# Kernel tuning notes

Hardware: AMD Instinct MI355X
Metric: run time of the kernel (lower is better)

## Reference

```python
import jax, jax.numpy as jnp
import numpy as np


def _maxpool2(x):
    # 2x2 max pool, stride 2; x: [B, C, H, W]
    B, C, H, W = x.shape
    return x.reshape(B, C, H // 2, 2, W // 2, 2).max(axis=(3, 5))


def setup_inputs() -> dict:
    key = jax.random.key(0)
    ks = jax.random.split(key, 6)
    B, C, H, W = 8, 256, 64, 64
    x = jax.random.normal(ks[0], (B, C, H, W), dtype=jnp.float32)
    w_theta = jax.random.normal(ks[1], (C // 8, C), dtype=jnp.float32) * (C ** -0.5)
    w_phi = jax.random.normal(ks[2], (C // 8, C), dtype=jnp.float32) * (C ** -0.5)
    w_g = jax.random.normal(ks[3], (C // 2, C), dtype=jnp.float32) * (C ** -0.5)
    w_o = jax.random.normal(ks[4], (C, C // 2), dtype=jnp.float32) * ((C // 2) ** -0.5)
    gamma = jnp.ones((), dtype=jnp.float32)
    return {"x": x, "w_theta": w_theta, "w_phi": w_phi, "w_g": w_g, "w_o": w_o, "gamma": gamma}


def reference(x, w_theta, w_phi, w_g, w_o, gamma):
    B, C, H, W = x.shape
    N = H * W
    # 1x1 convs are channel-mixing matmuls
    theta = jnp.einsum('oc,bchw->bohw', w_theta, x).reshape(B, C // 8, N)        # [B, C/8, N]
    phi = _maxpool2(jnp.einsum('oc,bchw->bohw', w_phi, x)).reshape(B, C // 8, N // 4)  # [B, C/8, N/4]
    g = _maxpool2(jnp.einsum('oc,bchw->bohw', w_g, x)).reshape(B, C // 2, N // 4)      # [B, C/2, N/4]
    # attention: softmax(theta^T phi) over pooled key axis
    beta = jax.nn.softmax(jnp.einsum('bcn,bcm->bnm', theta, phi), axis=-1)       # [B, N, N/4]
    o = jnp.einsum('bcm,bnm->bcn', g, beta).reshape(B, C // 2, H, W)             # [B, C/2, H, W]
    o = jnp.einsum('oc,bchw->bohw', w_o, o)                                      # [B, C, H, W]
    return gamma * o + x
```

## Files before the change

kernel.cpp:

```cpp
#include <hip/hip_runtime.h>

#define B_ 8
#define C_ 256
#define N_ 4096
#define CK 32
#define CG 128
#define M_ 1024

typedef __attribute__((ext_vector_type(8))) short bf16x8;
typedef __attribute__((ext_vector_type(4))) float f32x4;

__device__ __forceinline__ short f2bf(float f) {
  union { float f; unsigned u; } v; v.f = f;
  unsigned r = (v.u + 0x7FFF + ((v.u >> 16) & 1)) >> 16;
  return (short)r;
}
__device__ __forceinline__ int cvtpk(float lo, float hi) {
  int r;
  asm("v_cvt_pk_bf16_f32 %0, %1, %2" : "=v"(r) : "v"(lo), "v"(hi));
  return r;
}
__device__ __forceinline__ bf16x8 asbf(int4 v) {
  union { int4 i; bf16x8 b; } u; u.i = v; return u.b;
}
__device__ __forceinline__ void gload_lds16(const void* g, void* l) {
  __builtin_amdgcn_global_load_lds(
      (const __attribute__((address_space(1))) void*)g,
      (__attribute__((address_space(3))) void*)l, 16, 0, 0);
}

__global__ __launch_bounds__(512) void proj_kernel(const float* __restrict__ x,
                                                   const float* __restrict__ wt,
                                                   const float* __restrict__ wp,
                                                   const float* __restrict__ wg,
                                                   short* __restrict__ theta_t,
                                                   short* __restrict__ phi_t,
                                                   short* __restrict__ g_bf) {
  __shared__ __align__(16) short w_s[192 * 256];
  __shared__ __align__(16) short x_s[64 * 256];
  int tid = threadIdx.x;
  int bx = blockIdx.x, b = blockIdx.y;
  int t = bx >> 1, half = bx & 1;

#pragma unroll
  for (int rep = 0; rep < 12; ++rep) {
    int idx = rep * 512 + tid;
    int o = idx >> 5, gp = idx & 31;
    const float* src = (o < 32) ? (wt + o * 256)
                     : (o < 64) ? (wp + (o - 32) * 256)
                                : (wg + (o - 64) * 256);
    float4 f0 = *(const float4*)(src + gp * 8);
    float4 f1 = *(const float4*)(src + gp * 8 + 4);
    int4 pk;
    pk.x = cvtpk(f0.x, f0.y); pk.y = cvtpk(f0.z, f0.w);
    pk.z = cvtpk(f1.x, f1.y); pk.w = cvtpk(f1.z, f1.w);
    *(int4*)&w_s[o * 256 + ((gp ^ (o & 7)) * 8)] = pk;
  }
  {
    int l = tid & 63, cq = tid >> 6;
    int xoff = l >> 1, dy = l & 1;
    int n = t * 128 + dy * 64 + half * 32 + xoff;
    const float* xb = x + (size_t)b * C_ * N_ + n;
#pragma unroll
    for (int rep = 0; rep < 2; ++rep) {
      int ch = cq + rep * 8;
      int c0 = ch * 16;
      float f[16];
#pragma unroll
      for (int i = 0; i < 16; ++i) f[i] = xb[(size_t)(c0 + i) * N_];
      int4 pa, pb;
      pa.x = cvtpk(f[0], f[1]);   pa.y = cvtpk(f[2], f[3]);
      pa.z = cvtpk(f[4], f[5]);   pa.w = cvtpk(f[6], f[7]);
      pb.x = cvtpk(f[8], f[9]);   pb.y = cvtpk(f[10], f[11]);
      pb.z = cvtpk(f[12], f[13]); pb.w = cvtpk(f[14], f[15]);
      *(int4*)&x_s[l * 256 + (((2 * ch) ^ (l & 7)) * 8)] = pa;
      *(int4*)&x_s[l * 256 + (((2 * ch + 1) ^ (l & 7)) * 8)] = pb;
    }
  }
  __syncthreads();

  int lane = tid & 63, w = tid >> 6;
  int h = lane >> 4, q = lane & 15;
  int ns = w & 3, ow = w >> 2;
  f32x4 acc[6];
#pragma unroll
  for (int j = 0; j < 6; ++j) acc[j] = (f32x4){0.f, 0.f, 0.f, 0.f};

  int nl = 16 * ns + q;
#pragma unroll
  for (int ks = 0; ks < 8; ++ks) {
    bf16x8 bfr = *(const bf16x8*)&x_s[nl * 256 + (((4 * ks + h) ^ (nl & 7)) * 8)];
#pragma unroll
    for (int j = 0; j < 6; ++j) {
      int o = 16 * (6 * ow + j) + q;
      bf16x8 afr = *(const bf16x8*)&w_s[o * 256 + (((4 * ks + h) ^ (o & 7)) * 8)];
      acc[j] = __builtin_amdgcn_mfma_f32_16x16x32_bf16(afr, bfr, acc[j], 0, 0, 0);
    }
  }

  int xoff = nl >> 1, dy = nl & 1;
  int n = t * 128 + dy * 64 + half * 32 + xoff;
  int m = t * 32 + half * 16 + (nl >> 2);
  int mp = (m & ~31) | (((m >> 2) & 3) << 3) | (((m >> 4) & 1) << 2) | (m & 3);
#pragma unroll
  for (int j = 0; j < 6; ++j) {
    int ot = 6 * ow + j;
    if (ot < 2) {
      int2 pp;
      pp.x = cvtpk(acc[j][0], acc[j][1]);
      pp.y = cvtpk(acc[j][2], acc[j][3]);
      *(int2*)&theta_t[((size_t)b * N_ + n) * CK + ot * 16 + 4 * h] = pp;
    } else {
      float v[4];
#pragma unroll
      for (int r = 0; r < 4; ++r) {
        float vv = acc[j][r];
        vv = fmaxf(vv, __shfl_xor(vv, 1));
        vv = fmaxf(vv, __shfl_xor(vv, 2));
        v[r] = vv;
      }
      if ((nl & 3) == 0) {
        if (ot < 4) {
          int2 pp;
          pp.x = cvtpk(v[0], v[1]);
          pp.y = cvtpk(v[2], v[3]);
          *(int2*)&phi_t[((size_t)b * M_ + m) * CK + (ot - 2) * 16 + 4 * h] = pp;
        } else {
#pragma unroll
          for (int r = 0; r < 4; ++r) {
            int oc = (ot - 4) * 16 + 4 * h + r;
            g_bf[((size_t)b * CG + oc) * M_ + mp] = f2bf(v[r]);
          }
        }
      }
    }
  }
}

__global__ __launch_bounds__(128, 2) void attn_out_kernel(const short* __restrict__ theta_t,
                                                          const short* __restrict__ phi_t,
                                                          const short* __restrict__ g_bf,
                                                          const float* __restrict__ wo,
                                                          const float* __restrict__ x,
                                                          const float* __restrict__ gamma,
                                                          float* __restrict__ out) {
  __shared__ __align__(16) short lds[16384];
  short* g_s = lds;

  int tid = threadIdx.x;
  int lane = tid & 63, w = tid >> 6;
  int h = lane >> 4, q = lane & 15;
  int bid = blockIdx.x;
  int b = bid & 7, n0 = (bid >> 3) * 32;
  int n = n0 + 16 * w + q;
  float gm = gamma[0];

  bf16x8 qfrag = *(const bf16x8*)&theta_t[((size_t)b * N_ + n) * CK + 8 * h];

  f32x4 Oacc[8];
#pragma unroll
  for (int ct = 0; ct < 8; ++ct) Oacc[ct] = (f32x4){0.f, 0.f, 0.f, 0.f};
  float S = 0.f;
  const f32x4 zero4 = {0.f, 0.f, 0.f, 0.f};

  const short* phi_b = phi_t + (size_t)b * M_ * CK;
  const short* g_b = g_bf + (size_t)b * CG * M_;

  int srow = tid >> 3;
  int sgrp = (tid & 7) ^ (srow & 7);
  size_t srcoff = (size_t)srow * M_ + sgrp * 8;
  int wbase = tid & ~63;

  int4 pcur[4];
#pragma unroll
  for (int mt = 0; mt < 4; ++mt)
    pcur[mt] = *(const int4*)&phi_b[(16 * mt + q) * CK + 8 * h];
#pragma unroll
  for (int k = 0; k < 8; ++k)
    gload_lds16(g_b + (size_t)k * 16 * M_ + srcoff,
                &g_s[(k * 128 + wbase) * 8]);
  __syncthreads();

  for (int it = 0; it < 16; ++it) {
    int cur = it & 1;
    const short* g_c = g_s + cur * 8192;
    int4 pnxt[4];
    if (it < 15) {
      int m0n = (it + 1) * 64;
#pragma unroll
      for (int k = 0; k < 8; ++k)
        gload_lds16(g_b + (size_t)k * 16 * M_ + srcoff + m0n,
                    &g_s[(cur ^ 1) * 8192 + (k * 128 + wbase) * 8]);
#pragma unroll
      for (int mt = 0; mt < 4; ++mt)
        pnxt[mt] = *(const int4*)&phi_b[(m0n + 16 * mt + q) * CK + 8 * h];
    }

    f32x4 pt[4];
#pragma unroll
    for (int mt = 0; mt < 4; ++mt)
      pt[mt] = __builtin_amdgcn_mfma_f32_16x16x32_bf16(asbf(pcur[mt]), qfrag, zero4, 0, 0, 0);

    int2 pk[4];
#pragma unroll
    for (int mt = 0; mt < 4; ++mt) {
      float e0 = __expf(pt[mt][0]);
      float e1 = __expf(pt[mt][1]);
      float e2 = __expf(pt[mt][2]);
      float e3 = __expf(pt[mt][3]);
      S += (e0 + e1) + (e2 + e3);
      pk[mt].x = cvtpk(e0, e1);
      pk[mt].y = cvtpk(e2, e3);
    }

    __builtin_amdgcn_s_setprio(1);
#pragma unroll
    for (int kp = 0; kp < 2; ++kp) {
      int4 pfi;
      pfi.x = pk[2 * kp].x;     pfi.y = pk[2 * kp].y;
      pfi.z = pk[2 * kp + 1].x; pfi.w = pk[2 * kp + 1].y;
      bf16x8 pf = asbf(pfi);
#pragma unroll
      for (int ct = 0; ct < 8; ++ct) {
        bf16x8 vf = *(const bf16x8*)&g_c[(16 * ct + q) * 64 +
                                         (((4 * kp + h) ^ (q & 7)) * 8)];
        Oacc[ct] = __builtin_amdgcn_mfma_f32_16x16x32_bf16(vf, pf, Oacc[ct], 0, 0, 0);
      }
    }
    __builtin_amdgcn_s_setprio(0);

    if (it < 15) {
#pragma unroll
      for (int mt = 0; mt < 4; ++mt) pcur[mt] = pnxt[mt];
    }
    __syncthreads();
  }

  S += __shfl_xor(S, 16);
  S += __shfl_xor(S, 32);

  short* ot_s = lds;
  short* wo_s = lds + 4352;
  float rS = 1.f / S;
  int nloc = 16 * w + q;
#pragma unroll
  for (int ct = 0; ct < 8; ++ct) {
    int2 pp;
    pp.x = cvtpk(Oacc[ct][0] * rS, Oacc[ct][1] * rS);
    pp.y = cvtpk(Oacc[ct][2] * rS, Oacc[ct][3] * rS);
    *(int2*)&ot_s[nloc * 136 + 16 * ct + 4 * h] = pp;
  }

#pragma unroll
  for (int tq = 0; tq < 4; ++tq) {
#pragma unroll
    for (int rep = 0; rep < 8; ++rep) {
      int idx = rep * 128 + tid;
      int ol = idx >> 4, gp = idx & 15;
      const float* src = wo + (size_t)(64 * tq + ol) * 128 + gp * 8;
      float4 f0 = *(const float4*)src;
      float4 f1 = *(const float4*)(src + 4);
      int4 pk2;
      pk2.x = cvtpk(f0.x, f0.y); pk2.y = cvtpk(f0.z, f0.w);
      pk2.z = cvtpk(f1.x, f1.y); pk2.w = cvtpk(f1.z, f1.w);
      *(int4*)&wo_s[ol * 128 + ((gp ^ (ol & 7)) * 8)] = pk2;
    }
    __syncthreads();

    f32x4 acc[4];
#pragma unroll
    for (int j = 0; j < 4; ++j) acc[j] = (f32x4){0.f, 0.f, 0.f, 0.f};

#pragma unroll
    for (int ks = 0; ks < 4; ++ks) {
      bf16x8 bfr = *(const bf16x8*)&ot_s[(16 * w + q) * 136 + 32 * ks + 8 * h];
#pragma unroll
      for (int j = 0; j < 4; ++j) {
        int ol = 16 * j + q;
        bf16x8 afr = *(const bf16x8*)&wo_s[ol * 128 + (((4 * ks + h) ^ (ol & 7)) * 8)];
        acc[j] = __builtin_amdgcn_mfma_f32_16x16x32_bf16(afr, bfr, acc[j], 0, 0, 0);
      }
    }

#pragma unroll
    for (int j = 0; j < 4; ++j)
#pragma unroll
      for (int r = 0; r < 4; ++r) {
        int o = 64 * tq + 16 * j + 4 * h + r;
        size_t idx = ((size_t)b * C_ + o) * N_ + n;
        out[idx] = gm * acc[j][r] + x[idx];
      }
    __syncthreads();
  }
}

extern "C" void kernel_launch(void* const* d_in, const int* in_sizes, int n_in,
                              void* d_out, int out_size, void* d_ws, size_t ws_size,
                              hipStream_t stream) {
  const float* x = (const float*)d_in[0];
  const float* wt = (const float*)d_in[1];
  const float* wp = (const float*)d_in[2];
  const float* wg = (const float*)d_in[3];
  const float* wo = (const float*)d_in[4];
  const float* gamma = (const float*)d_in[5];
  float* out = (float*)d_out;

  short* theta_t = (short*)d_ws;
  short* phi_t = theta_t + (size_t)B_ * N_ * CK;
  short* g_bf = phi_t + (size_t)B_ * M_ * CK;

  proj_kernel<<<dim3(64, 8), 512, 0, stream>>>(x, wt, wp, wg, theta_t, phi_t, g_bf);
  attn_out_kernel<<<dim3(1024), 128, 0, stream>>>(theta_t, phi_t, g_bf, wo, x, gamma, out);
}
```

Baseline: 53.18 us.

## Split attention key range across wave groups with 512-thread blocks and LDS reduction

```diff
diff --git a/kernel.cpp b/kernel.cpp
--- a/kernel.cpp
+++ b/kernel.cpp
@@ -137,22 +137,22 @@
   }
 }
 
-__global__ __launch_bounds__(128, 2) void attn_out_kernel(const short* __restrict__ theta_t,
+__global__ __launch_bounds__(512, 4) void attn_out_kernel(const short* __restrict__ theta_t,
                                                           const short* __restrict__ phi_t,
                                                           const short* __restrict__ g_bf,
                                                           const float* __restrict__ wo,
                                                           const float* __restrict__ x,
                                                           const float* __restrict__ gamma,
                                                           float* __restrict__ out) {
-  __shared__ __align__(16) short lds[16384];
-  short* g_s = lds;
+  __shared__ __align__(16) short lds[32768];
 
   int tid = threadIdx.x;
   int lane = tid & 63, w = tid >> 6;
   int h = lane >> 4, q = lane & 15;
+  int w_n = w & 3, w_m = w >> 2;
   int bid = blockIdx.x;
-  int b = bid & 7, n0 = (bid >> 3) * 32;
-  int n = n0 + 16 * w + q;
+  int b = bid & 7, n0 = (bid >> 3) * 64;
+  int n = n0 + 16 * w_n + q;
   float gm = gamma[0];
 
   bf16x8 qfrag = *(const bf16x8*)&theta_t[((size_t)b * N_ + n) * CK + 8 * h];
@@ -166,34 +166,37 @@
   const short* phi_b = phi_t + (size_t)b * M_ * CK;
   const short* g_b = g_bf + (size_t)b * CG * M_;
 
-  int srow = tid >> 3;
-  int sgrp = (tid & 7) ^ (srow & 7);
-  size_t srcoff = (size_t)srow * M_ + sgrp * 8;
-  int wbase = tid & ~63;
+  int ht = tid & 255;
+  int srow = ht >> 3;
+  int sgrp = (ht & 7) ^ (srow & 7);
+  size_t srcoff = (size_t)srow * M_ + sgrp * 8 + (size_t)w_m * 512;
+  int wslot = ht & ~63;
+  short* gbase = lds + w_m * 16384;
+  int mbase = w_m * 512;
 
   int4 pcur[4];
 #pragma unroll
   for (int mt = 0; mt < 4; ++mt)
-    pcur[mt] = *(const int4*)&phi_b[(16 * mt + q) * CK + 8 * h];
-#pragma unroll
-  for (int k = 0; k < 8; ++k)
-    gload_lds16(g_b + (size_t)k * 16 * M_ + srcoff,
-                &g_s[(k * 128 + wbase) * 8]);
+    pcur[mt] = *(const int4*)&phi_b[(mbase + 16 * mt + q) * CK + 8 * h];
+#pragma unroll
+  for (int k = 0; k < 4; ++k)
+    gload_lds16(g_b + (size_t)k * 32 * M_ + srcoff,
+                &gbase[(k * 256 + wslot) * 8]);
   __syncthreads();
 
-  for (int it = 0; it < 16; ++it) {
+  for (int it = 0; it < 8; ++it) {
     int cur = it & 1;
-    const short* g_c = g_s + cur * 8192;
+    const short* g_c = gbase + cur * 8192;
     int4 pnxt[4];
-    if (it < 15) {
+    if (it < 7) {
       int m0n = (it + 1) * 64;
 #pragma unroll
-      for (int k = 0; k < 8; ++k)
-        gload_lds16(g_b + (size_t)k * 16 * M_ + srcoff + m0n,
-                    &g_s[(cur ^ 1) * 8192 + (k * 128 + wbase) * 8]);
+      for (int k = 0; k < 4; ++k)
+        gload_lds16(g_b + (size_t)k * 32 * M_ + srcoff + m0n,
+                    &gbase[(cur ^ 1) * 8192 + (k * 256 + wslot) * 8]);
 #pragma unroll
       for (int mt = 0; mt < 4; ++mt)
-        pnxt[mt] = *(const int4*)&phi_b[(m0n + 16 * mt + q) * CK + 8 * h];
+        pnxt[mt] = *(const int4*)&phi_b[(mbase + m0n + 16 * mt + q) * CK + 8 * h];
     }
 
     f32x4 pt[4];
@@ -229,7 +232,7 @@
     }
     __builtin_amdgcn_s_setprio(0);
 
-    if (it < 15) {
+    if (it < 7) {
 #pragma unroll
       for (int mt = 0; mt < 4; ++mt) pcur[mt] = pnxt[mt];
     }
@@ -239,23 +242,43 @@
   S += __shfl_xor(S, 16);
   S += __shfl_xor(S, 32);
 
+  float* otf = (float*)lds;
+  float* s_f = otf + 64 * 132;
+  int row = 16 * w_n + q;
+  if (w_m == 1) {
+#pragma unroll
+    for (int ct = 0; ct < 8; ++ct)
+      *(f32x4*)&otf[row * 132 + 16 * ct + 4 * h] = Oacc[ct];
+    if (h == 0) s_f[row] = S;
+  }
+  __syncthreads();
+  if (w_m == 0) {
+#pragma unroll
+    for (int ct = 0; ct < 8; ++ct)
+      Oacc[ct] += *(const f32x4*)&otf[row * 132 + 16 * ct + 4 * h];
+    S += s_f[row];
+  }
+  float rS = 1.f / S;
+  __syncthreads();
+
   short* ot_s = lds;
-  short* wo_s = lds + 4352;
-  float rS = 1.f / S;
-  int nloc = 16 * w + q;
-#pragma unroll
-  for (int ct = 0; ct < 8; ++ct) {
-    int2 pp;
-    pp.x = cvtpk(Oacc[ct][0] * rS, Oacc[ct][1] * rS);
-    pp.y = cvtpk(Oacc[ct][2] * rS, Oacc[ct][3] * rS);
-    *(int2*)&ot_s[nloc * 136 + 16 * ct + 4 * h] = pp;
-  }
-
+  short* wo_s = lds + 8704;
+  if (w_m == 0) {
+#pragma unroll
+    for (int ct = 0; ct < 8; ++ct) {
+      int2 pp;
+      pp.x = cvtpk(Oacc[ct][0] * rS, Oacc[ct][1] * rS);
+      pp.y = cvtpk(Oacc[ct][2] * rS, Oacc[ct][3] * rS);
+      *(int2*)&ot_s[row * 136 + 16 * ct + 4 * h] = pp;
+    }
+  }
+
+  int jj = w & 3, np = w >> 2;
 #pragma unroll
   for (int tq = 0; tq < 4; ++tq) {
 #pragma unroll
-    for (int rep = 0; rep < 8; ++rep) {
-      int idx = rep * 128 + tid;
+    for (int rep = 0; rep < 2; ++rep) {
+      int idx = rep * 512 + tid;
       int ol = idx >> 4, gp = idx & 15;
       const float* src = wo + (size_t)(64 * tq + ol) * 128 + gp * 8;
       float4 f0 = *(const float4*)src;
@@ -267,28 +290,27 @@
     }
     __syncthreads();
 
-    f32x4 acc[4];
-#pragma unroll
-    for (int j = 0; j < 4; ++j) acc[j] = (f32x4){0.f, 0.f, 0.f, 0.f};
-
+    f32x4 acc[2];
+    acc[0] = (f32x4){0.f, 0.f, 0.f, 0.f};
+    acc[1] = (f32x4){0.f, 0.f, 0.f, 0.f};
 #pragma unroll
     for (int ks = 0; ks < 4; ++ks) {
-      bf16x8 bfr = *(const bf16x8*)&ot_s[(16 * w + q) * 136 + 32 * ks + 8 * h];
-#pragma unroll
-      for (int j = 0; j < 4; ++j) {
-        int ol = 16 * j + q;
-        bf16x8 afr = *(const bf16x8*)&wo_s[ol * 128 + (((4 * ks + h) ^ (ol & 7)) * 8)];
-        acc[j] = __builtin_amdgcn_mfma_f32_16x16x32_bf16(afr, bfr, acc[j], 0, 0, 0);
-      }
-    }
-
-#pragma unroll
-    for (int j = 0; j < 4; ++j)
+      bf16x8 bfr0 = *(const bf16x8*)&ot_s[(16 * (2 * np) + q) * 136 + 32 * ks + 8 * h];
+      bf16x8 bfr1 = *(const bf16x8*)&ot_s[(16 * (2 * np + 1) + q) * 136 + 32 * ks + 8 * h];
+      int ol = 16 * jj + q;
+      bf16x8 afr = *(const bf16x8*)&wo_s[ol * 128 + (((4 * ks + h) ^ (ol & 7)) * 8)];
+      acc[0] = __builtin_amdgcn_mfma_f32_16x16x32_bf16(afr, bfr0, acc[0], 0, 0, 0);
+      acc[1] = __builtin_amdgcn_mfma_f32_16x16x32_bf16(afr, bfr1, acc[1], 0, 0, 0);
+    }
+
+#pragma unroll
+    for (int i = 0; i < 2; ++i)
 #pragma unroll
       for (int r = 0; r < 4; ++r) {
-        int o = 64 * tq + 16 * j + 4 * h + r;
-        size_t idx = ((size_t)b * C_ + o) * N_ + n;
-        out[idx] = gm * acc[j][r] + x[idx];
+        int o = 64 * tq + 16 * jj + 4 * h + r;
+        int nn = n0 + 16 * (2 * np + i) + q;
+        size_t idx = ((size_t)b * C_ + o) * N_ + nn;
+        out[idx] = gm * acc[i][r] + x[idx];
       }
     __syncthreads();
   }
@@ -310,5 +332,5 @@
   short* g_bf = phi_t + (size_t)B_ * M_ * CK;
 
   proj_kernel<<<dim3(64, 8), 512, 0, stream>>>(x, wt, wp, wg, theta_t, phi_t, g_bf);
-  attn_out_kernel<<<dim3(1024), 128, 0, stream>>>(theta_t, phi_t, g_bf, wo, x, gamma, out);
-}
+  attn_out_kernel<<<dim3(512), 512, 0, stream>>>(theta_t, phi_t, g_bf, wo, x, gamma, out);
+}
```

After: 49.47 us. 1.08x faster.
